# Kernel optimization log

Measured on AMD Instinct MI355X. Metric: run time of the kernel, lower is better.

The kernel has to match this reference:

```python
import jax, jax.numpy as jnp
import numpy as np

B, E, F_DIM, D = 32, 16, 64, 512  # batch, extra dim, fea_dim, input_dim
EXP = 4                            # feed-forward expansion
EPS = 1e-5


def _layernorm(x, g, b):
    m = jnp.mean(x, axis=-1, keepdims=True)
    v = jnp.mean(jnp.square(x - m), axis=-1, keepdims=True)
    return (x - m) * jax.lax.rsqrt(v + EPS) * g + b


def setup_inputs() -> dict:
    key = jax.random.key(0)
    ks = jax.random.split(key, 12)
    s = 1.0 / np.sqrt(D)
    inp = {
        "x": jax.random.normal(ks[0], (B, E, F_DIM, D), jnp.float32),
        "ln1_g": jnp.ones((D,), jnp.float32),
        "ln1_b": jnp.zeros((D,), jnp.float32),
        "Wq": jax.random.uniform(ks[1], (D, D), jnp.float32, -s, s),
        "bq": jax.random.uniform(ks[2], (D,), jnp.float32, -s, s),
        "Wk": jax.random.uniform(ks[3], (D, D), jnp.float32, -s, s),
        "bk": jax.random.uniform(ks[4], (D,), jnp.float32, -s, s),
        "Wv": jax.random.uniform(ks[5], (D, D), jnp.float32, -s, s),
        "bv": jax.random.uniform(ks[6], (D,), jnp.float32, -s, s),
        "wn_g": jnp.ones((F_DIM,), jnp.float32),
        "wn_b": jnp.zeros((F_DIM,), jnp.float32),
        "ln2_g": jnp.ones((D,), jnp.float32),
        "ln2_b": jnp.zeros((D,), jnp.float32),
        "W1": jax.random.uniform(ks[7], (D, EXP * D), jnp.float32, -s, s),
        "b1": jax.random.uniform(ks[8], (EXP * D,), jnp.float32, -s, s),
        "W2": jax.random.uniform(ks[9], (EXP * D, D), jnp.float32, -1.0 / np.sqrt(EXP * D), 1.0 / np.sqrt(EXP * D)),
        "b2": jax.random.uniform(ks[10], (D,), jnp.float32, -1.0 / np.sqrt(EXP * D), 1.0 / np.sqrt(EXP * D)),
    }
    return inp


def reference(x, ln1_g, ln1_b, Wq, bq, Wk, bk, Wv, bv, wn_g, wn_b, ln2_g, ln2_b, W1, b1, W2, b2):
    # --- Residual 1: LN -> feature multi-head attention (dropout = identity) ---
    h = _layernorm(x, ln1_g, ln1_b)                       # [B,E,F,D]
    q = h @ Wq + bq
    k = h @ Wk + bk
    v = h @ Wv + bv
    energy = jnp.einsum('beqd,bekd->beqk', q, k)          # [B,E,F,F]
    # LayerNorm over the key axis of the raw scores (the fusion-breaking op)
    energy = _layernorm(energy, wn_g, wn_b)
    att = jax.nn.softmax(energy / jnp.sqrt(jnp.float32(D)), axis=-1)
    attn_out = jnp.einsum('beal,belv->beav', att, v)      # [B,E,F,D]
    x = x + attn_out
    # --- Residual 2: LN -> FFN (Linear -> Linear, no activation) ---
    h2 = _layernorm(x, ln2_g, ln2_b)
    ff = (h2 @ W1 + b1) @ W2 + b2
    return x + ff
```

## Files before the change

### kernel.cpp

```cpp
#include <hip/hip_runtime.h>
#include <hip/hip_bf16.h>


#define D_DIM 512
#define NROWS 32768
#define NBE   512

typedef __attribute__((ext_vector_type(8))) short bf16x8;
typedef __attribute__((ext_vector_type(4))) float f32x4;

typedef const __attribute__((address_space(1))) unsigned g_u32;
typedef __attribute__((address_space(3))) unsigned lds_u32;

__device__ __forceinline__ short f2bf(float f) {
  union { float f; unsigned u; } c; c.f = f;
  unsigned u = c.u;
  unsigned r = (u + 0x7FFFu + ((u >> 16) & 1u)) >> 16;
  return (short)r;
}
__device__ __forceinline__ float bf2f(short s) {
  union { unsigned u; float f; } c; c.u = ((unsigned)(unsigned short)s) << 16;
  return c.f;
}

__global__ __launch_bounds__(256) void wconvT(const float* __restrict__ W,
                                              short* __restrict__ Wt,
                                              int K, int N) {
  __shared__ float tile[32][33];
  const int t = threadIdx.x;
  const int r  = t >> 3;
  const int c4 = (t & 7) * 4;
  const long k0 = (long)blockIdx.y * 32;
  const long n0 = (long)blockIdx.x * 32;
  float4 v = *(const float4*)&W[(k0 + r) * N + n0 + c4];
  tile[r][c4 + 0] = v.x; tile[r][c4 + 1] = v.y;
  tile[r][c4 + 2] = v.z; tile[r][c4 + 3] = v.w;
  __syncthreads();
  union { short sh[4]; int2 v; } o;
#pragma unroll
  for (int j = 0; j < 4; ++j) o.sh[j] = f2bf(tile[c4 + j][r]);
  *(int2*)&Wt[(n0 + r) * K + k0 + c4] = o.v;
}

__global__ __launch_bounds__(256) void ln_kernel(const float* __restrict__ x,
                                                 const float* __restrict__ gam,
                                                 const float* __restrict__ bet,
                                                 short* __restrict__ h) {
  const int t = threadIdx.x;
  const long row = (long)blockIdx.x * 4 + (t >> 6);
  const int lane = t & 63;
  const float* xr = x + row * D_DIM + lane * 8;
  float4 a = *(const float4*)xr;
  float4 b = *(const float4*)(xr + 4);
  float xs[8] = {a.x, a.y, a.z, a.w, b.x, b.y, b.z, b.w};
  float s = 0.f, ss = 0.f;
#pragma unroll
  for (int j = 0; j < 8; ++j) { s += xs[j]; ss += xs[j] * xs[j]; }
#pragma unroll
  for (int m = 1; m < 64; m <<= 1) {
    s  += __shfl_xor(s, m);
    ss += __shfl_xor(ss, m);
  }
  float mean = s * (1.f / D_DIM);
  float var  = ss * (1.f / D_DIM) - mean * mean;
  float rstd = rsqrtf(var + 1e-5f);
  union { short sh[8]; int4 v; } o;
#pragma unroll
  for (int j = 0; j < 8; ++j) {
    int d = lane * 8 + j;
    o.sh[j] = f2bf((xs[j] - mean) * rstd * gam[d] + bet[d]);
  }
  *(int4*)&h[row * D_DIM + lane * 8] = o.v;
}

template <int OUT_BF16, int RESID>
__global__ __launch_bounds__(256) void gemm128(
    const short* __restrict__ A, const short* __restrict__ Bt,
    const float* __restrict__ bias0, const float* __restrict__ bias1,
    const float* __restrict__ bias2,
    void* __restrict__ out0, void* __restrict__ out1, void* __restrict__ out2,
    const float* __restrict__ resid, int K, int nsplit) {
  __shared__ short As[128 * 32];
  __shared__ short Bs[128 * 32];
  const int t = threadIdx.x;
  const int wave = t >> 6, lane = t & 63;
  const int lr = lane & 15, g = lane >> 4;
  const int wr = wave >> 1, wc = wave & 1;

  const int gx = gridDim.x;
  const int nwg = gx * gridDim.y;
  const int hid = blockIdx.y * gx + blockIdx.x;
  const int lid = (hid & 7) * (nwg >> 3) + (hid >> 3);
  const int m0 = (lid / gx) * 128;
  const int n0 = (lid % gx) * 128;

  const int seg = n0 / nsplit;
  const int ncol0 = n0 - seg * nsplit;
  const float* bias = seg == 0 ? bias0 : (seg == 1 ? bias1 : bias2);
  void* outp = seg == 0 ? out0 : (seg == 1 ? out1 : out2);

  const int crow = lane >> 2;
  const int ccol = (lane & 3) * 8;

  f32x4 acc[4][4];
  const f32x4 vzero = {0.f, 0.f, 0.f, 0.f};
#pragma unroll
  for (int mi = 0; mi < 4; ++mi)
#pragma unroll
    for (int ni = 0; ni < 4; ++ni) acc[mi][ni] = vzero;

  for (int k0 = 0; k0 < K; k0 += 32) {
#pragma unroll
    for (int i = 0; i < 2; ++i) {
      const int c = wave * 2 + i;
      const int row = c * 16 + crow;
      __builtin_amdgcn_global_load_lds(
          (g_u32*)&A[(long)(m0 + row) * K + k0 + ccol],
          (lds_u32*)&As[c * 512], 16, 0, 0);
      __builtin_amdgcn_global_load_lds(
          (g_u32*)&Bt[(long)(n0 + row) * K + k0 + ccol],
          (lds_u32*)&Bs[c * 512], 16, 0, 0);
    }
    __syncthreads();
    bf16x8 af[4], bf[4];
#pragma unroll
    for (int mi = 0; mi < 4; ++mi)
      af[mi] = *(const bf16x8*)&As[(wr * 64 + mi * 16 + lr) * 32 + g * 8];
#pragma unroll
    for (int ni = 0; ni < 4; ++ni)
      bf[ni] = *(const bf16x8*)&Bs[(wc * 64 + ni * 16 + lr) * 32 + g * 8];
#pragma unroll
    for (int mi = 0; mi < 4; ++mi)
#pragma unroll
      for (int ni = 0; ni < 4; ++ni)
        acc[mi][ni] = __builtin_amdgcn_mfma_f32_16x16x32_bf16(af[mi], bf[ni], acc[mi][ni], 0, 0, 0);
    __syncthreads();
  }

#pragma unroll
  for (int ni = 0; ni < 4; ++ni) {
    const int col = ncol0 + wc * 64 + ni * 16 + lr;
    const float bv = bias[col];
#pragma unroll
    for (int mi = 0; mi < 4; ++mi) {
#pragma unroll
      for (int r = 0; r < 4; ++r) {
        const long row = m0 + wr * 64 + mi * 16 + g * 4 + r;
        float val = acc[mi][ni][r] + bv;
        if (RESID) val += resid[row * (long)nsplit + col];
        if (OUT_BF16) ((short*)outp)[row * (long)nsplit + col] = f2bf(val);
        else          ((float*)outp)[row * (long)nsplit + col] = val;
      }
    }
  }
}

__global__ __launch_bounds__(256) void attn_kernel(
    const short* __restrict__ q, const short* __restrict__ k,
    const short* __restrict__ v, const float* __restrict__ x,
    const float* __restrict__ wn_g, const float* __restrict__ wn_b,
    const float* __restrict__ ln2_g, const float* __restrict__ ln2_b,
    float* __restrict__ x1, short* __restrict__ h2) {
  __shared__ float att_s[64][68];
  const int t = threadIdx.x;
  const int wave = t >> 6, lane = t & 63;
  const int lr = lane & 15, g = lane >> 4;
  const long base = (long)blockIdx.x * 64;
  const long qoff = base * D_DIM;

  const f32x4 vzero = {0.f, 0.f, 0.f, 0.f};
  f32x4 acc[4];
#pragma unroll
  for (int nt = 0; nt < 4; ++nt) acc[nt] = vzero;

  for (int ks = 0; ks < 16; ++ks) {
    const int kc = ks * 32 + g * 8;
    bf16x8 afr = *(const bf16x8*)&q[qoff + (long)(wave * 16 + lr) * D_DIM + kc];
#pragma unroll
    for (int nt = 0; nt < 4; ++nt) {
      bf16x8 bfr = *(const bf16x8*)&k[qoff + (long)(nt * 16 + lr) * D_DIM + kc];
      acc[nt] = __builtin_amdgcn_mfma_f32_16x16x32_bf16(afr, bfr, acc[nt], 0, 0, 0);
    }
  }

  const float scale = 0.044194173824159216f;
#pragma unroll
  for (int r = 0; r < 4; ++r) {
    float s = 0.f, ss = 0.f;
#pragma unroll
    for (int nt = 0; nt < 4; ++nt) { float e = acc[nt][r]; s += e; ss += e * e; }
#pragma unroll
    for (int m = 1; m < 16; m <<= 1) { s += __shfl_xor(s, m); ss += __shfl_xor(ss, m); }
    float mean = s * (1.f / 64);
    float var  = ss * (1.f / 64) - mean * mean;
    float rstd = rsqrtf(var + 1e-5f);
    float e[4]; float mx = -1e30f;
#pragma unroll
    for (int nt = 0; nt < 4; ++nt) {
      int col = nt * 16 + lr;
      e[nt] = ((acc[nt][r] - mean) * rstd * wn_g[col] + wn_b[col]) * scale;
      mx = fmaxf(mx, e[nt]);
    }
#pragma unroll
    for (int m = 1; m < 16; m <<= 1) mx = fmaxf(mx, __shfl_xor(mx, m));
    float se = 0.f;
#pragma unroll
    for (int nt = 0; nt < 4; ++nt) { e[nt] = expf(e[nt] - mx); se += e[nt]; }
#pragma unroll
    for (int m = 1; m < 16; m <<= 1) se += __shfl_xor(se, m);
    float inv = 1.f / se;
#pragma unroll
    for (int nt = 0; nt < 4; ++nt)
      att_s[wave * 16 + 4 * g + r][nt * 16 + lr] = e[nt] * inv;
  }
  __syncthreads();

  const int d0 = lane * 8;
  float accp[16][8];
#pragma unroll
  for (int qi = 0; qi < 16; ++qi)
#pragma unroll
    for (int j = 0; j < 8; ++j) accp[qi][j] = 0.f;

  for (int kk0 = 0; kk0 < 64; kk0 += 4) {
    float vf[4][8];
#pragma unroll
    for (int kc = 0; kc < 4; ++kc) {
      bf16x8 vv = *(const bf16x8*)&v[qoff + (long)(kk0 + kc) * D_DIM + d0];
#pragma unroll
      for (int j = 0; j < 8; ++j) vf[kc][j] = bf2f(vv[j]);
    }
#pragma unroll
    for (int qi = 0; qi < 16; ++qi) {
      float4 a4 = *(const float4*)&att_s[wave * 16 + qi][kk0];
#pragma unroll
      for (int j = 0; j < 8; ++j) {
        accp[qi][j] += a4.x * vf[0][j];
        accp[qi][j] += a4.y * vf[1][j];
        accp[qi][j] += a4.z * vf[2][j];
        accp[qi][j] += a4.w * vf[3][j];
      }
    }
  }

  float g2v[8], b2v[8];
#pragma unroll
  for (int j = 0; j < 8; ++j) { g2v[j] = ln2_g[d0 + j]; b2v[j] = ln2_b[d0 + j]; }

#pragma unroll
  for (int qi = 0; qi < 16; ++qi) {
    const long row = base + wave * 16 + qi;
    const float* xr = x + row * D_DIM + d0;
    float4 x0 = *(const float4*)xr;
    float4 xb = *(const float4*)(xr + 4);
    accp[qi][0] += x0.x; accp[qi][1] += x0.y;
    accp[qi][2] += x0.z; accp[qi][3] += x0.w;
    accp[qi][4] += xb.x; accp[qi][5] += xb.y;
    accp[qi][6] += xb.z; accp[qi][7] += xb.w;
    float* po = x1 + row * D_DIM + d0;
    *(float4*)po       = make_float4(accp[qi][0], accp[qi][1], accp[qi][2], accp[qi][3]);
    *(float4*)(po + 4) = make_float4(accp[qi][4], accp[qi][5], accp[qi][6], accp[qi][7]);
    float s = 0.f, ss = 0.f;
#pragma unroll
    for (int j = 0; j < 8; ++j) { s += accp[qi][j]; ss += accp[qi][j] * accp[qi][j]; }
#pragma unroll
    for (int m = 1; m < 64; m <<= 1) { s += __shfl_xor(s, m); ss += __shfl_xor(ss, m); }
    float mean = s * (1.f / D_DIM);
    float var  = ss * (1.f / D_DIM) - mean * mean;
    float rstd = rsqrtf(var + 1e-5f);
    union { short sh[8]; int4 v; } o;
#pragma unroll
    for (int j = 0; j < 8; ++j)
      o.sh[j] = f2bf((accp[qi][j] - mean) * rstd * g2v[j] + b2v[j]);
    *(int4*)&h2[row * D_DIM + d0] = o.v;
  }
}

extern "C" void kernel_launch(void* const* d_in, const int* in_sizes, int n_in,
                              void* d_out, int out_size, void* d_ws, size_t ws_size,
                              hipStream_t stream) {
  (void)in_sizes; (void)n_in; (void)out_size; (void)ws_size;
  const float* x     = (const float*)d_in[0];
  const float* ln1_g = (const float*)d_in[1];
  const float* ln1_b = (const float*)d_in[2];
  const float* Wq    = (const float*)d_in[3];
  const float* bq    = (const float*)d_in[4];
  const float* Wk    = (const float*)d_in[5];
  const float* bk    = (const float*)d_in[6];
  const float* Wv    = (const float*)d_in[7];
  const float* bv    = (const float*)d_in[8];
  const float* wn_g  = (const float*)d_in[9];
  const float* wn_b  = (const float*)d_in[10];
  const float* ln2_g = (const float*)d_in[11];
  const float* ln2_b = (const float*)d_in[12];
  const float* W1    = (const float*)d_in[13];
  const float* b1    = (const float*)d_in[14];
  const float* W2    = (const float*)d_in[15];
  const float* b2    = (const float*)d_in[16];
  float* out = (float*)d_out;

  char* ws = (char*)d_ws;
  short* h   = (short*)(ws);
  short* qb  = (short*)(ws + (size_t)32  * 1024 * 1024);
  short* kb  = (short*)(ws + (size_t)64  * 1024 * 1024);
  short* vb  = (short*)(ws + (size_t)96  * 1024 * 1024);
  short* ff1 = (short*)(ws + (size_t)32  * 1024 * 1024);
  short* Wqt = (short*)(ws + (size_t)160 * 1024 * 1024);
  short* Wkt = Wqt + 512 * 512;
  short* Wvt = Wkt + 512 * 512;
  short* W1t = Wvt + 512 * 512;
  short* W2t = W1t + 512 * 2048;

  wconvT<<<dim3(512 / 32, 512 / 32),  256, 0, stream>>>(Wq, Wqt, 512, 512);
  wconvT<<<dim3(512 / 32, 512 / 32),  256, 0, stream>>>(Wk, Wkt, 512, 512);
  wconvT<<<dim3(512 / 32, 512 / 32),  256, 0, stream>>>(Wv, Wvt, 512, 512);
  wconvT<<<dim3(2048 / 32, 512 / 32), 256, 0, stream>>>(W1, W1t, 512, 2048);
  wconvT<<<dim3(512 / 32, 2048 / 32), 256, 0, stream>>>(W2, W2t, 2048, 512);

  ln_kernel<<<NROWS / 4, 256, 0, stream>>>(x, ln1_g, ln1_b, h);

  dim3 gqkv(1536 / 128, NROWS / 128);
  gemm128<1, 0><<<gqkv, 256, 0, stream>>>(h, Wqt, bq, bk, bv,
                                          qb, kb, vb, nullptr, 512, 512);

  attn_kernel<<<NBE, 256, 0, stream>>>(qb, kb, vb, x, wn_g, wn_b,
                                       ln2_g, ln2_b, out, h);

  dim3 gff1(2048 / 128, NROWS / 128);
  gemm128<1, 0><<<gff1, 256, 0, stream>>>(h, W1t, b1, b1, b1,
                                          ff1, ff1, ff1, nullptr, 512, 2048);

  dim3 gff2(512 / 128, NROWS / 128);
  gemm128<0, 1><<<gff2, 256, 0, stream>>>(ff1, W2t, b2, b2, b2,
                                          out, out, out, out, 2048, 512);
}
```

Before: 571.7 us.

## Double-buffer GEMM LDS tiles and use fragment-ordered LDS layout

```diff
diff --git a/kernel.cpp b/kernel.cpp
--- a/kernel.cpp
+++ b/kernel.cpp
@@ -80,8 +80,8 @@
     const float* __restrict__ bias2,
     void* __restrict__ out0, void* __restrict__ out1, void* __restrict__ out2,
     const float* __restrict__ resid, int K, int nsplit) {
-  __shared__ short As[128 * 32];
-  __shared__ short Bs[128 * 32];
+  __shared__ short As[2][8 * 512];
+  __shared__ short Bs[2][8 * 512];
   const int t = threadIdx.x;
   const int wave = t >> 6, lane = t & 63;
   const int lr = lane & 15, g = lane >> 4;
@@ -99,8 +99,26 @@
   const float* bias = seg == 0 ? bias0 : (seg == 1 ? bias1 : bias2);
   void* outp = seg == 0 ? out0 : (seg == 1 ? out1 : out2);
 
-  const int crow = lane >> 2;
-  const int ccol = (lane & 3) * 8;
+  const int srow = lane & 15;
+  const int scol = (lane >> 4) * 8;
+  const short* gA0 = &A[(long)(m0 + wave * 32 + srow) * K + scol];
+  const short* gB0 = &Bt[(long)(n0 + wave * 32 + srow) * K + scol];
+  const long rstep = 16L * K;
+
+  const int nsteps = K >> 5;
+  int cur = 0;
+
+#define STAGE(bufi, kk)                                                        \
+  do {                                                                         \
+    __builtin_amdgcn_global_load_lds((g_u32*)(gA0 + (kk)),                     \
+        (lds_u32*)&As[bufi][(wave * 2) * 512], 16, 0, 0);                      \
+    __builtin_amdgcn_global_load_lds((g_u32*)(gA0 + rstep + (kk)),             \
+        (lds_u32*)&As[bufi][(wave * 2 + 1) * 512], 16, 0, 0);                  \
+    __builtin_amdgcn_global_load_lds((g_u32*)(gB0 + (kk)),                     \
+        (lds_u32*)&Bs[bufi][(wave * 2) * 512], 16, 0, 0);                      \
+    __builtin_amdgcn_global_load_lds((g_u32*)(gB0 + rstep + (kk)),             \
+        (lds_u32*)&Bs[bufi][(wave * 2 + 1) * 512], 16, 0, 0);                  \
+  } while (0)
 
   f32x4 acc[4][4];
   const f32x4 vzero = {0.f, 0.f, 0.f, 0.f};
@@ -109,33 +127,32 @@
 #pragma unroll
     for (int ni = 0; ni < 4; ++ni) acc[mi][ni] = vzero;
 
-  for (int k0 = 0; k0 < K; k0 += 32) {
-#pragma unroll
-    for (int i = 0; i < 2; ++i) {
-      const int c = wave * 2 + i;
-      const int row = c * 16 + crow;
-      __builtin_amdgcn_global_load_lds(
-          (g_u32*)&A[(long)(m0 + row) * K + k0 + ccol],
-          (lds_u32*)&As[c * 512], 16, 0, 0);
-      __builtin_amdgcn_global_load_lds(
-          (g_u32*)&Bt[(long)(n0 + row) * K + k0 + ccol],
-          (lds_u32*)&Bs[c * 512], 16, 0, 0);
-    }
-    __syncthreads();
-    bf16x8 af[4], bf[4];
+  STAGE(0, 0);
+  __syncthreads();
+
+  const int fo = lane * 8;
+  for (int st = 0; st < nsteps; ++st) {
+    if (st + 1 < nsteps) STAGE(cur ^ 1, (st + 1) * 32);
+    const short* sA = &As[cur][0];
+    const short* sB = &Bs[cur][0];
+    bf16x8 af[4], bfr[4];
 #pragma unroll
     for (int mi = 0; mi < 4; ++mi)
-      af[mi] = *(const bf16x8*)&As[(wr * 64 + mi * 16 + lr) * 32 + g * 8];
+      af[mi] = *(const bf16x8*)&sA[(wr * 4 + mi) * 512 + fo];
 #pragma unroll
     for (int ni = 0; ni < 4; ++ni)
-      bf[ni] = *(const bf16x8*)&Bs[(wc * 64 + ni * 16 + lr) * 32 + g * 8];
+      bfr[ni] = *(const bf16x8*)&sB[(wc * 4 + ni) * 512 + fo];
 #pragma unroll
     for (int mi = 0; mi < 4; ++mi)
 #pragma unroll
       for (int ni = 0; ni < 4; ++ni)
-        acc[mi][ni] = __builtin_amdgcn_mfma_f32_16x16x32_bf16(af[mi], bf[ni], acc[mi][ni], 0, 0, 0);
-    __syncthreads();
-  }
+        acc[mi][ni] = __builtin_amdgcn_mfma_f32_16x16x32_bf16(af[mi], bfr[ni], acc[mi][ni], 0, 0, 0);
+    if (st + 1 < nsteps) {
+      __syncthreads();
+      cur ^= 1;
+    }
+  }
+#undef STAGE
 
 #pragma unroll
   for (int ni = 0; ni < 4; ++ni) {
```

Result: slower. 645.6 us (+12.9%).
